# Performance work log

Measured on AMD Instinct MI355X. Metric: run time of the kernel, lower is better.

The kernel has to match this reference:

```python
import jax, jax.numpy as jnp
import numpy as np

B, T = 64, 2000
Q_DIM, M_DIM, A_DIM = 1024, 512, 128
FILTERS, KSIZE = 32, 31


def setup_inputs() -> dict:
    key = jax.random.key(0)
    ks = jax.random.split(key, 12)
    s = lambda *sh: 1.0 / np.sqrt(sh[0])
    inp = {
        "query": jax.random.normal(ks[0], (B, Q_DIM), jnp.float32),
        "memory": jax.random.normal(ks[1], (B, T, M_DIM), jnp.float32),
        "alignments_cat": jax.random.uniform(ks[2], (B, T, 2), jnp.float32),
        "mask": jnp.ones((B, T), jnp.bool_),
        # parameters
        "Wq": jax.random.normal(ks[3], (Q_DIM, A_DIM), jnp.float32) * s(Q_DIM),
        "bq": jnp.zeros((A_DIM,), jnp.float32),
        "Wm": jax.random.normal(ks[4], (M_DIM, A_DIM), jnp.float32) * s(M_DIM),
        "bm": jnp.zeros((A_DIM,), jnp.float32),
        # conv kernel: [out_ch=FILTERS, in_ch=2, K]
        "conv_w": jax.random.normal(ks[5], (FILTERS, 2, KSIZE), jnp.float32) * s(2 * KSIZE),
        "Wl": jax.random.normal(ks[6], (FILTERS, A_DIM), jnp.float32) * s(FILTERS),
        "v_w": jax.random.normal(ks[7], (A_DIM, 1), jnp.float32) * s(A_DIM),
        "v_b": jnp.zeros((1,), jnp.float32),
    }
    return inp


def reference(query, memory, alignments_cat, mask, Wq, bq, Wm, bm, conv_w, Wl, v_w, v_b):
    # processed memory: [B, T, A]
    pm = jnp.einsum("btd,da->bta", memory, Wm) + bm
    # processed query: [B, 1, A]
    pq = (query @ Wq + bq)[:, None, :]
    # location features: conv over time on [B, 2, T] -> [B, F, T] (SAME padding)
    x = alignments_cat.transpose(0, 2, 1)  # [B, 2, T]
    pad = (KSIZE - 1) // 2
    loc = jax.lax.conv_general_dilated(
        x, conv_w, window_strides=(1,), padding=[(pad, pad)],
        dimension_numbers=("NCH", "OIH", "NCH"))  # [B, F, T]
    pl = jnp.einsum("bft,fa->bta", loc, Wl)  # [B, T, A]
    # additive attention score: [B, T]
    score = (jnp.tanh(pq + pm + pl) @ v_w)[..., 0] + v_b[0]
    score = jnp.where(mask, score, -jnp.inf)
    alignment = jax.nn.softmax(score, axis=-1)  # [B, T]
    context = jnp.einsum("bt,btd->bd", alignment, memory)  # [B, M_DIM]
    return context, alignment
```

## Files before the change

### kernel.cpp

```cpp
#include <hip/hip_runtime.h>
#include <math.h>

#define B_SZ 64
#define T_SZ 2000
#define QD   1024
#define MD   512
#define AD   128
#define NF   32
#define KS   31
#define CPAD 15

#define BT   128
#define ACS_W (BT + 2 * CPAD)

typedef short bf16x8 __attribute__((ext_vector_type(8)));
typedef float floatx16 __attribute__((ext_vector_type(16)));
typedef unsigned int uintx4 __attribute__((ext_vector_type(4)));

__device__ __forceinline__ unsigned short bf1(float f) {
  unsigned u = __float_as_uint(f);
  unsigned r = u + 0x7FFFu + ((u >> 16) & 1u);
  return (unsigned short)(r >> 16);
}
__device__ __forceinline__ unsigned pk2(float a, float b) {
  return (unsigned)bf1(a) | ((unsigned)bf1(b) << 16);
}
__device__ __forceinline__ bf16x8 pack8(float4 lo, float4 hi) {
  uintx4 u;
  u.x = pk2(lo.x, lo.y); u.y = pk2(lo.z, lo.w);
  u.z = pk2(hi.x, hi.y); u.w = pk2(hi.z, hi.w);
  return __builtin_bit_cast(bf16x8, u);
}

#define GLD16(g, l)                                                      \
  __builtin_amdgcn_global_load_lds(                                      \
      (const __attribute__((address_space(1))) void*)(g),                \
      (__attribute__((address_space(3))) void*)(l), 16, 0, 0)

__global__ __launch_bounds__(256) void wmtx_kernel(
    const float* __restrict__ Wm, const float* __restrict__ Wl,
    const float* __restrict__ convw, unsigned short* __restrict__ WmtX) {
  const int sid = blockIdx.x * 256 + threadIdx.x;
  const int kt = sid >> 10;
  const int s = sid & 1023;
  const int ks = s >> 8, ct = (s >> 6) & 3, kh = (s >> 5) & 1, ln = s & 31;
  const int a = ct * 32 + ln;
  float v[8];
  if (kt < 8) {
    const int k0 = kt * 64 + ks * 16 + kh * 8;
#pragma unroll
    for (int j = 0; j < 8; ++j) v[j] = Wm[(k0 + j) * AD + a];
  } else {
#pragma unroll
    for (int j = 0; j < 8; ++j) {
      const int kI = ks * 16 + kh * 8 + j;
      float acc = 0.f;
      if (kI < 62) {
        const int c = (kI >= 31) ? 1 : 0;
        const int kk = kI - c * 31;
        for (int f = 0; f < NF; ++f)
          acc += Wl[f * AD + a] * convw[f * (2 * KS) + c * KS + kk];
      }
      v[j] = acc;
    }
  }
  uintx4 u;
  u.x = pk2(v[0], v[1]); u.y = pk2(v[2], v[3]);
  u.z = pk2(v[4], v[5]); u.w = pk2(v[6], v[7]);
  *reinterpret_cast<uintx4*>(WmtX + (size_t)sid * 8) = u;
}

__global__ __launch_bounds__(128) void pq_kernel(const float* __restrict__ query,
                                                 const float* __restrict__ Wq,
                                                 const float* __restrict__ bq,
                                                 float* __restrict__ pq8) {
  const int b = blockIdx.x, h = blockIdx.y, a = threadIdx.x;
  __shared__ float q[128];
  q[a] = query[b * QD + h * 128 + a];
  __syncthreads();
  float s = (h == 0) ? bq[a] : 0.f;
#pragma unroll 8
  for (int d = 0; d < 128; ++d) s += q[d] * Wq[(h * 128 + d) * AD + a];
  pq8[(h * B_SZ + b) * AD + a] = s;
}

__global__ __launch_bounds__(256, 2) void score_kernel(
    const float* __restrict__ memory, const float* __restrict__ ac,
    const unsigned short* __restrict__ WmtX, const float* __restrict__ bm,
    const float* __restrict__ vw, const float* __restrict__ vb,
    const float* __restrict__ pq8, float* __restrict__ score) {
  __shared__ unsigned short Bbuf[2][8192];
  __shared__ float acs[2 * ACS_W];
  __shared__ float pqs[AD], bms[AD], vws[AD];

  const int tid = threadIdx.x;
  const int b = blockIdx.y;
  const int t0 = blockIdx.x * BT;
  const int lane = tid & 63, wv = tid >> 6;
  const int ln = lane & 31, kh = lane >> 5;

  int trow = t0 + wv * 32 + ln;
  if (trow > T_SZ - 1) trow = T_SZ - 1;
  const float* arow = memory + ((size_t)b * T_SZ + trow) * MD;

  {
    const char* g = (const char*)WmtX;
    char* lb = (char*)&Bbuf[0][0];
#pragma unroll
    for (int i = 0; i < 4; ++i) {
      const int slot = wv * 256 + i * 64 + lane;
      GLD16(g + slot * 16, lb + (wv * 256 + i * 64) * 16);
    }
  }
  float4 A[2][8];
#pragma unroll
  for (int ks = 0; ks < 4; ++ks) {
    const float* p = arow + ks * 16 + kh * 8;
    A[0][2 * ks] = *reinterpret_cast<const float4*>(p);
    A[0][2 * ks + 1] = *reinterpret_cast<const float4*>(p + 4);
  }

  for (int i = tid; i < AD; i += 256) {
    float s = 0.f;
#pragma unroll
    for (int h = 0; h < 8; ++h) s += pq8[(h * B_SZ + b) * AD + i];
    pqs[i] = s;
    bms[i] = bm[i];
    vws[i] = vw[i];
  }
  for (int i = tid; i < 2 * ACS_W; i += 256) {
    const int c = (i >= ACS_W);
    const int j = i - c * ACS_W;
    const int t = t0 - CPAD + j;
    acs[i] = (t >= 0 && t < T_SZ) ? ac[((size_t)b * T_SZ + t) * 2 + c] : 0.f;
  }

  floatx16 acc[4];
#pragma unroll
  for (int ct = 0; ct < 4; ++ct)
#pragma unroll
    for (int i = 0; i < 16; ++i) acc[ct][i] = 0.f;

#pragma unroll
  for (int kt = 0; kt < 8; ++kt) {
    __syncthreads();
    {
      const char* g = (const char*)WmtX + (size_t)(kt + 1) * 16384;
      char* lb = (char*)&Bbuf[(kt + 1) & 1][0];
#pragma unroll
      for (int i = 0; i < 4; ++i) {
        const int slot = wv * 256 + i * 64 + lane;
        GLD16(g + slot * 16, lb + (wv * 256 + i * 64) * 16);
      }
    }
    if (kt < 7) {
#pragma unroll
      for (int ks = 0; ks < 4; ++ks) {
        const float* p = arow + (kt + 1) * 64 + ks * 16 + kh * 8;
        A[(kt + 1) & 1][2 * ks] = *reinterpret_cast<const float4*>(p);
        A[(kt + 1) & 1][2 * ks + 1] = *reinterpret_cast<const float4*>(p + 4);
      }
    }
    const unsigned short* Bb = &Bbuf[kt & 1][0];
#pragma unroll
    for (int ks = 0; ks < 4; ++ks) {
      bf16x8 af = pack8(A[kt & 1][2 * ks], A[kt & 1][2 * ks + 1]);
#pragma unroll
      for (int ct = 0; ct < 4; ++ct) {
        bf16x8 bf = *reinterpret_cast<const bf16x8*>(
            Bb + (ks * 256 + ct * 64 + kh * 32 + ln) * 8);
        acc[ct] = __builtin_amdgcn_mfma_f32_32x32x16_bf16(af, bf, acc[ct], 0, 0, 0);
      }
    }
  }

  __syncthreads();
  {
    const unsigned short* Bb = &Bbuf[0][0];
    const float* a0 = acs;
    const float* a1 = acs + ACS_W;
    const int tt = wv * 32 + ln;
#pragma unroll
    for (int ks = 0; ks < 4; ++ks) {
      float v[8];
#pragma unroll
      for (int j = 0; j < 8; ++j) {
        const int kI = ks * 16 + kh * 8 + j;
        float x = 0.f;
        if (kI < 31) x = a0[tt + kI];
        else if (kI < 62) x = a1[tt + kI - 31];
        v[j] = x;
      }
      bf16x8 af = pack8(make_float4(v[0], v[1], v[2], v[3]),
                        make_float4(v[4], v[5], v[6], v[7]));
#pragma unroll
      for (int ct = 0; ct < 4; ++ct) {
        bf16x8 bf = *reinterpret_cast<const bf16x8*>(
            Bb + (ks * 256 + ct * 64 + kh * 32 + ln) * 8);
        acc[ct] = __builtin_amdgcn_mfma_f32_32x32x16_bf16(af, bf, acc[ct], 0, 0, 0);
      }
    }
  }

  const float vb0 = vb[0];
  float rsum[16];
#pragma unroll
  for (int r = 0; r < 16; ++r) rsum[r] = 0.f;
#pragma unroll
  for (int ct = 0; ct < 4; ++ct) {
    const int col = ct * 32 + ln;
    const float add = pqs[col] + bms[col];
    const float vwc = vws[col];
#pragma unroll
    for (int r = 0; r < 16; ++r) {
      float s = acc[ct][r] + add;
      float e = __expf(2.f * s);
      rsum[r] += (1.f - 2.f / (e + 1.f)) * vwc;
    }
  }
#pragma unroll
  for (int m = 1; m <= 16; m <<= 1)
#pragma unroll
    for (int r = 0; r < 16; ++r) rsum[r] += __shfl_xor(rsum[r], m, 64);
  if (ln == 0) {
#pragma unroll
    for (int r = 0; r < 16; ++r) {
      const int row = wv * 32 + (r & 3) + 8 * (r >> 2) + 4 * kh;
      const int t = t0 + row;
      if (t < T_SZ) score[(size_t)b * T_SZ + t] = rsum[r] + vb0;
    }
  }
}

__global__ __launch_bounds__(256) void softmax_kernel(
    const float* __restrict__ score, float* __restrict__ align) {
  const int b = blockIdx.x, tid = threadIdx.x;
  __shared__ float sm[8];
  float lmax = -1e30f;
  for (int t = tid; t < T_SZ; t += 256) lmax = fmaxf(lmax, score[b * T_SZ + t]);
  for (int o = 32; o > 0; o >>= 1) lmax = fmaxf(lmax, __shfl_down(lmax, o, 64));
  if ((tid & 63) == 0) sm[tid >> 6] = lmax;
  __syncthreads();
  if (tid == 0) {
    float m = sm[0];
    for (int i = 1; i < 4; ++i) m = fmaxf(m, sm[i]);
    sm[0] = m;
  }
  __syncthreads();
  const float m = sm[0];
  float lsum = 0.f;
  for (int t = tid; t < T_SZ; t += 256) lsum += __expf(score[b * T_SZ + t] - m);
  for (int o = 32; o > 0; o >>= 1) lsum += __shfl_down(lsum, o, 64);
  if ((tid & 63) == 0) sm[4 + (tid >> 6)] = lsum;
  __syncthreads();
  if (tid == 0) {
    float s = 0.f;
    for (int i = 0; i < 4; ++i) s += sm[4 + i];
    sm[4] = s;
  }
  __syncthreads();
  const float inv = 1.f / sm[4];
  for (int t = tid; t < T_SZ; t += 256)
    align[b * T_SZ + t] = __expf(score[b * T_SZ + t] - m) * inv;
}

__global__ __launch_bounds__(256) void context_kernel(
    const float* __restrict__ align, const float* __restrict__ memory,
    float* __restrict__ context) {
  const int b = blockIdx.y, slice = blockIdx.x;
  const int tid = threadIdx.x;
  const int half = tid >> 7;
  const int d4 = (tid & 127) * 4;
  const int tbeg = slice * 100, tend = tbeg + 100;
  float4 acc = make_float4(0.f, 0.f, 0.f, 0.f);
#pragma unroll 5
  for (int t = tbeg + half; t < tend; t += 2) {
    const float al = align[b * T_SZ + t];
    const float4 v =
        *reinterpret_cast<const float4*>(memory + ((size_t)b * T_SZ + t) * MD + d4);
    acc.x += al * v.x; acc.y += al * v.y; acc.z += al * v.z; acc.w += al * v.w;
  }
  float* cp = context + b * MD + d4;
  atomicAdd(cp + 0, acc.x);
  atomicAdd(cp + 1, acc.y);
  atomicAdd(cp + 2, acc.z);
  atomicAdd(cp + 3, acc.w);
}

extern "C" void kernel_launch(void* const* d_in, const int* in_sizes, int n_in,
                              void* d_out, int out_size, void* d_ws, size_t ws_size,
                              hipStream_t stream) {
  const float* query = (const float*)d_in[0];
  const float* memory = (const float*)d_in[1];
  const float* ac = (const float*)d_in[2];
  const float* Wq = (const float*)d_in[4];
  const float* bq = (const float*)d_in[5];
  const float* Wm = (const float*)d_in[6];
  const float* bm = (const float*)d_in[7];
  const float* convw = (const float*)d_in[8];
  const float* Wl = (const float*)d_in[9];
  const float* vw = (const float*)d_in[10];
  const float* vb = (const float*)d_in[11];

  float* context = (float*)d_out;
  float* align = (float*)d_out + B_SZ * MD;
  unsigned short* WmtX = (unsigned short*)align;
  float* pq8 = align + 36864;
  float* score = (float*)d_ws;

  wmtx_kernel<<<36, 256, 0, stream>>>(Wm, Wl, convw, WmtX);

  dim3 gpq(B_SZ, 8);
  pq_kernel<<<gpq, 128, 0, stream>>>(query, Wq, bq, pq8);

  dim3 gs((T_SZ + BT - 1) / BT, B_SZ);
  score_kernel<<<gs, 256, 0, stream>>>(memory, ac, WmtX, bm, vw, vb, pq8, score);

  softmax_kernel<<<B_SZ, 256, 0, stream>>>(score, align);

  hipMemsetAsync(context, 0, B_SZ * MD * sizeof(float), stream);

  dim3 gc(20, B_SZ);
  context_kernel<<<gc, 256, 0, stream>>>(align, memory, context);
}
```

Measured before the change: 455.5 us.

## Fuse context accumulation into score kernel using unnormalized exp weights

The score kernel now computes exp(score) directly, with no max subtraction, and uses those weights to accumulate the weighted sum of the memory tile it already touched into context via atomics. A small normalize kernel then divides context and alignment by the per-batch sum. This removes the separate softmax pass and the second full read of memory in the context kernel. Skipping the max subtraction risks overflow if scores are large; here they are bounded by the tanh and v_w magnitudes. The memory tile is likely still in cache when it is re-read.

```diff
diff --git a/kernel.cpp b/kernel.cpp
--- a/kernel.cpp
+++ b/kernel.cpp
@@ -88,10 +88,12 @@
     const float* __restrict__ memory, const float* __restrict__ ac,
     const unsigned short* __restrict__ WmtX, const float* __restrict__ bm,
     const float* __restrict__ vw, const float* __restrict__ vb,
-    const float* __restrict__ pq8, float* __restrict__ score) {
+    const float* __restrict__ pq8, float* __restrict__ wout,
+    float* __restrict__ Nacc) {
   __shared__ unsigned short Bbuf[2][8192];
   __shared__ float acs[2 * ACS_W];
   __shared__ float pqs[AD], bms[AD], vws[AD];
+  __shared__ float wlds[BT];
 
   const int tid = threadIdx.x;
   const int b = blockIdx.y;
@@ -222,69 +224,64 @@
   for (int m = 1; m <= 16; m <<= 1)
 #pragma unroll
     for (int r = 0; r < 16; ++r) rsum[r] += __shfl_xor(rsum[r], m, 64);
+
   if (ln == 0) {
 #pragma unroll
     for (int r = 0; r < 16; ++r) {
       const int row = wv * 32 + (r & 3) + 8 * (r >> 2) + 4 * kh;
       const int t = t0 + row;
-      if (t < T_SZ) score[(size_t)b * T_SZ + t] = rsum[r] + vb0;
-    }
-  }
-}
-
-__global__ __launch_bounds__(256) void softmax_kernel(
-    const float* __restrict__ score, float* __restrict__ align) {
-  const int b = blockIdx.x, tid = threadIdx.x;
-  __shared__ float sm[8];
-  float lmax = -1e30f;
-  for (int t = tid; t < T_SZ; t += 256) lmax = fmaxf(lmax, score[b * T_SZ + t]);
-  for (int o = 32; o > 0; o >>= 1) lmax = fmaxf(lmax, __shfl_down(lmax, o, 64));
-  if ((tid & 63) == 0) sm[tid >> 6] = lmax;
+      float wr = 0.f;
+      if (t < T_SZ) {
+        wr = __expf(rsum[r] + vb0);
+        wout[(size_t)b * T_SZ + t] = wr;
+      }
+      wlds[row] = wr;
+    }
+  }
   __syncthreads();
-  if (tid == 0) {
-    float m = sm[0];
-    for (int i = 1; i < 4; ++i) m = fmaxf(m, sm[i]);
-    sm[0] = m;
-  }
+
+  {
+    const int h = tid >> 7;
+    const int d4 = (tid & 127) * 4;
+    const float* mb = memory + (size_t)b * T_SZ * MD + d4;
+    float4 a4 = make_float4(0.f, 0.f, 0.f, 0.f);
+#pragma unroll 8
+    for (int r = 0; r < 64; ++r) {
+      const int row = h * 64 + r;
+      int t = t0 + row;
+      if (t > T_SZ - 1) t = T_SZ - 1;
+      const float wr = wlds[row];
+      const float4 v = *reinterpret_cast<const float4*>(mb + (size_t)t * MD);
+      a4.x += wr * v.x; a4.y += wr * v.y; a4.z += wr * v.z; a4.w += wr * v.w;
+    }
+    float* np = Nacc + b * MD + d4;
+    atomicAdd(np + 0, a4.x);
+    atomicAdd(np + 1, a4.y);
+    atomicAdd(np + 2, a4.z);
+    atomicAdd(np + 3, a4.w);
+  }
+}
+
+__global__ __launch_bounds__(256) void normalize_kernel(
+    const float* __restrict__ w, float* __restrict__ context,
+    float* __restrict__ align) {
+  const int b = blockIdx.x, part = blockIdx.y, tid = threadIdx.x;
+  __shared__ float red[4];
+  float z = 0.f;
+  for (int t = tid; t < T_SZ; t += 256) z += w[(size_t)b * T_SZ + t];
+  for (int o = 32; o > 0; o >>= 1) z += __shfl_down(z, o, 64);
+  if ((tid & 63) == 0) red[tid >> 6] = z;
   __syncthreads();
-  const float m = sm[0];
-  float lsum = 0.f;
-  for (int t = tid; t < T_SZ; t += 256) lsum += __expf(score[b * T_SZ + t] - m);
-  for (int o = 32; o > 0; o >>= 1) lsum += __shfl_down(lsum, o, 64);
-  if ((tid & 63) == 0) sm[4 + (tid >> 6)] = lsum;
-  __syncthreads();
-  if (tid == 0) {
-    float s = 0.f;
-    for (int i = 0; i < 4; ++i) s += sm[4 + i];
-    sm[4] = s;
-  }
-  __syncthreads();
-  const float inv = 1.f / sm[4];
-  for (int t = tid; t < T_SZ; t += 256)
-    align[b * T_SZ + t] = __expf(score[b * T_SZ + t] - m) * inv;
-}
-
-__global__ __launch_bounds__(256) void context_kernel(
-    const float* __restrict__ align, const float* __restrict__ memory,
-    float* __restrict__ context) {
-  const int b = blockIdx.y, slice = blockIdx.x;
-  const int tid = threadIdx.x;
-  const int half = tid >> 7;
-  const int d4 = (tid & 127) * 4;
-  const int tbeg = slice * 100, tend = tbeg + 100;
-  float4 acc = make_float4(0.f, 0.f, 0.f, 0.f);
-#pragma unroll 5
-  for (int t = tbeg + half; t < tend; t += 2) {
-    const float al = align[b * T_SZ + t];
-    const float4 v =
-        *reinterpret_cast<const float4*>(memory + ((size_t)b * T_SZ + t) * MD + d4);
-    acc.x += al * v.x; acc.y += al * v.y; acc.z += al * v.z; acc.w += al * v.w;
-  }
-  float* cp = context + b * MD + d4;
-  atomicAdd(cp + 0, acc.x);
-  atomicAdd(cp + 1, acc.y);
-  atomicAdd(cp + 2, acc.z);
-  atomicAdd(cp + 3, acc.w);
+  const float invZ = 1.f / (red[0] + red[1] + red[2] + red[3]);
+  if (part == 0) {
+    for (int i = tid; i < MD; i += 256) context[b * MD + i] *= invZ;
+  } else {
+    const int tb = (part - 1) * 500;
+    for (int i = tid; i < 500; i += 256) {
+      const int t = tb + i;
+      align[(size_t)b * T_SZ + t] = w[(size_t)b * T_SZ + t] * invZ;
+    }
+  }
 }
 
 extern "C" void kernel_launch(void* const* d_in, const int* in_sizes, int n_in,
@@ -306,7 +303,9 @@
   float* align = (float*)d_out + B_SZ * MD;
   unsigned short* WmtX = (unsigned short*)align;
   float* pq8 = align + 36864;
-  float* score = (float*)d_ws;
+  float* wbuf = (float*)d_ws;
+
+  hipMemsetAsync(context, 0, B_SZ * MD * sizeof(float), stream);
 
   wmtx_kernel<<<36, 256, 0, stream>>>(Wm, Wl, convw, WmtX);
 
@@ -314,12 +313,9 @@
   pq_kernel<<<gpq, 128, 0, stream>>>(query, Wq, bq, pq8);
 
   dim3 gs((T_SZ + BT - 1) / BT, B_SZ);
-  score_kernel<<<gs, 256, 0, stream>>>(memory, ac, WmtX, bm, vw, vb, pq8, score);
-
-  softmax_kernel<<<B_SZ, 256, 0, stream>>>(score, align);
-
-  hipMemsetAsync(context, 0, B_SZ * MD * sizeof(float), stream);
-
-  dim3 gc(20, B_SZ);
-  context_kernel<<<gc, 256, 0, stream>>>(align, memory, context);
-}
+  score_kernel<<<gs, 256, 0, stream>>>(memory, ac, WmtX, bm, vw, vb, pq8, wbuf,
+                                       context);
+
+  dim3 gn(B_SZ, 5);
+  normalize_kernel<<<gn, 256, 0, stream>>>(wbuf, context, align);
+}
```

Result: faster. 440.2 us (-3.4%).
